# Optimization experiments

Hardware: AMD Instinct MI355X
Metric: run time of the kernel (lower is better)

## Reference

```python
import jax, jax.numpy as jnp
import numpy as np

B, S, L, H, N_ITEMS = 16, 20, 64, 768, 50000  # sessions, max items/session, tokens/item, hidden, catalog
T = S * L
TEMP = 0.05       # config.temp
PAD_POS = 50      # pad item position id (see torch code)
EPS = 1e-8        # torch CosineSimilarity eps


def setup_inputs() -> dict:
    key = jax.random.key(0)
    k1, k2, k3, k4 = jax.random.split(key, 4)
    hidden = jax.random.normal(k1, (B, T, H), jnp.float32)
    emb = jax.random.normal(k2, (N_ITEMS, H), jnp.float32)
    # item position ids: each item's L tokens share position 1..S; padded items -> 50
    pos = np.tile(np.repeat(np.arange(1, S + 1), L)[None, :], (B, 1))  # [B,T]
    sess_len = np.asarray(jax.random.randint(k3, (B,), S // 2, S + 1))  # items per session
    item_idx = np.repeat(np.arange(S), L)[None, :]                      # [1,T]
    pos = np.where(item_idx < sess_len[:, None], pos, PAD_POS).astype(np.int32)
    attn = (pos != PAD_POS).astype(np.int32)
    attrs = np.asarray(jax.random.randint(k4, (B, T), 0, 4)).astype(np.int32)
    return {
        "hidden_states": hidden,
        "item_embedding": emb,
        "attention_mask": jnp.asarray(attn),
        "item_position_ids": jnp.asarray(pos),
        "attr_type_ids": jnp.asarray(attrs),
    }


def reference(hidden_states, item_embedding, attention_mask, item_position_ids, attr_type_ids):
    # --- RecformerPooler (pooler_type='item'): nan-mean pool tokens per item ---
    item_ids = jnp.arange(1, S + 1, dtype=item_position_ids.dtype)
    mask = item_position_ids[:, None, :] == item_ids[None, :, None]      # [B,S,T]
    counts = mask.sum(-1)                                                # [B,S]
    valid = counts > 0                                                   # items present in session
    maskf = mask.astype(hidden_states.dtype)
    pooled = jnp.einsum('bst,bth->bsh', maskf, hidden_states)
    pooled = pooled / jnp.maximum(counts, 1)[..., None].astype(hidden_states.dtype)
    # (torch produces NaN rows for invalid items; we carry `valid` instead)

    # --- Similarity: cosine / temp vs full item catalog ---
    pn = jnp.maximum(jnp.linalg.norm(pooled, axis=-1, keepdims=True), EPS)
    en = jnp.maximum(jnp.linalg.norm(item_embedding, axis=-1, keepdims=True), EPS)
    sim = jnp.einsum('bsh,nh->bns', pooled / pn, item_embedding / en) / TEMP  # [B,N,S]

    # --- reduce_session('maxsim'): NaN -> -inf, max over session items ---
    sim = jnp.where(valid[:, None, :], sim, -jnp.inf)
    scores = sim.max(axis=-1)  # [B, N]; trailing mean over attr dim (size 1) is identity
    return scores
```

## Files before the change

kernel.cpp:

```cpp
#include <hip/hip_runtime.h>

#define B_ 16
#define S_ 20
#define L_ 64
#define T_ 1280
#define H_ 768
#define NITEMS 50000
#define TEMP 0.05f
#define EPSN 1e-8f

#define BM 320
#define BN 128
#define BK 32
#define NKT (H_ / BK)

typedef __attribute__((ext_vector_type(8))) short short8;
typedef __attribute__((ext_vector_type(4))) short short4v;
typedef __attribute__((ext_vector_type(4))) float f32x4;

__device__ __forceinline__ unsigned short f2bf(float f) {
    unsigned int u = __float_as_uint(f);
    u = u + 0x7FFFu + ((u >> 16) & 1u);
    return (unsigned short)(u >> 16);
}

typedef __attribute__((address_space(3))) void lds_void;
typedef const __attribute__((address_space(1))) void gbl_void;
__device__ __forceinline__ void load_lds16(const void* g, void* l) {
    __builtin_amdgcn_global_load_lds((gbl_void*)g, (lds_void*)l, 16, 0, 0);
}

__global__ __launch_bounds__(192) void pool_kernel(const float* __restrict__ hidden,
                                                   const int* __restrict__ pos,
                                                   unsigned short* __restrict__ A,
                                                   int* __restrict__ valid) {
    const int row = blockIdx.x;
    const int b = row / S_, s = row % S_;
    const int tid = threadIdx.x;

    __shared__ float wgt[L_];
    __shared__ int cntS;
    __shared__ float red[3];

    const int* pbase = pos + b * T_ + s * L_;
    if (tid < L_) {
        const int match = (pbase[tid] == s + 1) ? 1 : 0;
        unsigned long long bal = __ballot(match);
        wgt[tid] = match ? 1.0f : 0.0f;
        if (tid == 0) cntS = (int)__popcll(bal);
    }
    __syncthreads();

    const int cnt = cntS;
    const float inv = 1.0f / (float)(cnt > 0 ? cnt : 1);
    const float* hbase = hidden + ((size_t)b * T_ + (size_t)s * L_) * H_ + tid * 4;

    float a0 = 0.f, a1 = 0.f, a2 = 0.f, a3 = 0.f;
#pragma unroll 8
    for (int t = 0; t < L_; ++t) {
        const float w = wgt[t];
        const float4 v = *reinterpret_cast<const float4*>(hbase + (size_t)t * H_);
        a0 += w * v.x; a1 += w * v.y; a2 += w * v.z; a3 += w * v.w;
    }
    a0 *= inv; a1 *= inv; a2 *= inv; a3 *= inv;

    float ss = a0 * a0 + a1 * a1 + a2 * a2 + a3 * a3;
#pragma unroll
    for (int off = 32; off; off >>= 1) ss += __shfl_xor(ss, off, 64);
    const int wave = tid >> 6, lane = tid & 63;
    if (lane == 0) red[wave] = ss;
    __syncthreads();
    const float tot = red[0] + red[1] + red[2];
    const float scale = 1.0f / (fmaxf(sqrtf(tot), EPSN) * TEMP);

    short4v w4;
    w4[0] = (short)f2bf(a0 * scale);
    w4[1] = (short)f2bf(a1 * scale);
    w4[2] = (short)f2bf(a2 * scale);
    w4[3] = (short)f2bf(a3 * scale);
    *reinterpret_cast<short4v*>(A + (size_t)row * H_ + tid * 4) = w4;
    if (tid == 0) valid[row] = (cnt > 0) ? 1 : 0;
}

__global__ __launch_bounds__(256, 2) void gemm_kernel(const float* __restrict__ emb,
                                                      const unsigned short* __restrict__ A,
                                                      const int* __restrict__ valid,
                                                      float* __restrict__ out) {
    const int n0 = blockIdx.x * BN;
    const int tid = threadIdx.x;
    const int wave = tid >> 6, lane = tid & 63, quad = lane >> 4, lq = lane & 15;

    __shared__ alignas(16) short As[2][BM * BK];
    __shared__ alignas(16) float Bs[2][BN * BK];
    __shared__ float sEn[BN];
    __shared__ int sMask[B_];

    if (tid < B_) {
        int m = 0;
        for (int s = 0; s < S_; ++s) m |= (valid[tid * S_ + s] ? 1 : 0) << s;
        sMask[tid] = m;
    }

    const unsigned short* aSrc = A + (size_t)(tid >> 2) * H_ + (tid & 3) * 8;
    const float* bSrc[4];
#pragma unroll
    for (int i = 0; i < 4; ++i) {
        int r = n0 + (tid >> 3) + i * 32;
        if (r > NITEMS - 1) r = NITEMS - 1;
        bSrc[i] = emb + (size_t)r * H_ + (tid & 7) * 4;
    }

#pragma unroll
    for (int i = 0; i < 5; ++i)
        load_lds16(aSrc + i * 64 * H_, (char*)(&As[0][0]) + tid * 16 + i * 4096);
#pragma unroll
    for (int i = 0; i < 4; ++i)
        load_lds16(bSrc[i], (char*)(&Bs[0][0]) + tid * 16 + i * 4096);

    float rowSq = 0.f;
    f32x4 acc[20][2];
#pragma unroll
    for (int i = 0; i < 20; ++i) {
        acc[i][0] = (f32x4)0.f;
        acc[i][1] = (f32x4)0.f;
    }

    int cur = 0;
    for (int kt = 0; kt < NKT; ++kt) {
        __syncthreads();
        if (kt + 1 < NKT) {
            const int k0 = (kt + 1) * BK;
#pragma unroll
            for (int i = 0; i < 5; ++i)
                load_lds16(aSrc + k0 + i * 64 * H_,
                           (char*)(&As[cur ^ 1][0]) + tid * 16 + i * 4096);
#pragma unroll
            for (int i = 0; i < 4; ++i)
                load_lds16(bSrc[i] + k0,
                           (char*)(&Bs[cur ^ 1][0]) + tid * 16 + i * 4096);
        }

        {
            const float* ep = &Bs[cur][(tid >> 1) * BK + (tid & 1) * 16];
#pragma unroll
            for (int i = 0; i < 4; ++i) {
                const float4 v = *reinterpret_cast<const float4*>(ep + i * 4);
                rowSq += v.x * v.x + v.y * v.y + v.z * v.z + v.w * v.w;
            }
        }

        short8 bF[2];
#pragma unroll
        for (int nf = 0; nf < 2; ++nf) {
            const float* bp = &Bs[cur][(wave * 32 + nf * 16 + lq) * BK + quad * 8];
            const float4 x = *reinterpret_cast<const float4*>(bp);
            const float4 y = *reinterpret_cast<const float4*>(bp + 4);
            short8 f;
            f[0] = (short)f2bf(x.x); f[1] = (short)f2bf(x.y);
            f[2] = (short)f2bf(x.z); f[3] = (short)f2bf(x.w);
            f[4] = (short)f2bf(y.x); f[5] = (short)f2bf(y.y);
            f[6] = (short)f2bf(y.z); f[7] = (short)f2bf(y.w);
            bF[nf] = f;
        }

#pragma unroll
        for (int mf = 0; mf < 20; ++mf) {
            const short8 aF =
                *reinterpret_cast<const short8*>(&As[cur][(mf * 16 + lq) * BK + quad * 8]);
            acc[mf][0] = __builtin_amdgcn_mfma_f32_16x16x32_bf16(aF, bF[0], acc[mf][0], 0, 0, 0);
            acc[mf][1] = __builtin_amdgcn_mfma_f32_16x16x32_bf16(aF, bF[1], acc[mf][1], 0, 0, 0);
        }
        cur ^= 1;
    }

    rowSq += __shfl_xor(rowSq, 1, 64);
    if (!(tid & 1)) sEn[tid >> 1] = fmaxf(sqrtf(rowSq), EPSN);
    __syncthreads();

#pragma unroll
    for (int nf = 0; nf < 2; ++nf) {
        const int ncol = wave * 32 + nf * 16 + lq;
        const int n = n0 + ncol;
        if (n >= NITEMS) continue;
        const float inv_en = 1.0f / sEn[ncol];
#pragma unroll
        for (int bb = 0; bb < B_; ++bb) {
            const int rLo = bb * S_;
            const int msk = sMask[bb];
            float lm = -__builtin_inff();
            const int mfLo = rLo >> 4;
            const int mfHi = (rLo + S_ - 1) >> 4;
#pragma unroll
            for (int mf = mfLo; mf <= mfHi; ++mf)
#pragma unroll
                for (int e = 0; e < 4; ++e) {
                    const int r = mf * 16 + quad * 4 + e;
                    const unsigned off = (unsigned)(r - rLo);
                    const bool ok = (off < (unsigned)S_) && ((msk >> off) & 1);
                    lm = ok ? fmaxf(lm, acc[mf][nf][e]) : lm;
                }
            lm = fmaxf(lm, __shfl_xor(lm, 16, 64));
            lm = fmaxf(lm, __shfl_xor(lm, 32, 64));
            if (quad == 0)
                out[(size_t)bb * NITEMS + n] = lm * inv_en;
        }
    }
}

extern "C" void kernel_launch(void* const* d_in, const int* in_sizes, int n_in,
                              void* d_out, int out_size, void* d_ws, size_t ws_size,
                              hipStream_t stream) {
    const float* hidden = (const float*)d_in[0];
    const float* emb    = (const float*)d_in[1];
    const int*   pos    = (const int*)d_in[3];
    float* out = (float*)d_out;

    unsigned short* Abf = (unsigned short*)d_ws;
    int* valid = (int*)((char*)d_ws + (size_t)320 * 768 * 2);

    pool_kernel<<<dim3(320), dim3(192), 0, stream>>>(hidden, pos, Abf, valid);
    gemm_kernel<<<dim3((NITEMS + BN - 1) / BN), dim3(256), 0, stream>>>(emb, Abf, valid, out);
}
```

Before: 299.0 us.

## Halve N tile, convert embeddings to bf16 before LDS, split waves over M

The embedding tile now goes through registers: each thread loads fp32 values, adds them to the row norm, converts them to bf16 and writes them to LDS, prefetching one k-step ahead. Before, fp32 was copied straight to LDS and each wave converted its fragments on every use. BN drops from 128 to 64 and the wave decomposition changes from splitting N to splitting M (80 rows per wave, 5x4 fragments), so each wave handles 4 sessions in the epilogue. This cuts LDS footprint and per-thread conversion work and doubles the number of blocks. In exchange, A-tile reuse per embedding row is lower and the synchronous global loads now sit in the main loop.

```diff
diff --git a/kernel.cpp b/kernel.cpp
--- a/kernel.cpp
+++ b/kernel.cpp
@@ -10,7 +10,7 @@
 #define EPSN 1e-8f
 
 #define BM 320
-#define BN 128
+#define BN 64
 #define BK 32
 #define NKT (H_ / BK)
 
@@ -91,7 +91,7 @@
     const int wave = tid >> 6, lane = tid & 63, quad = lane >> 4, lq = lane & 15;
 
     __shared__ alignas(16) short As[2][BM * BK];
-    __shared__ alignas(16) float Bs[2][BN * BK];
+    __shared__ alignas(16) short Bs[2][BN * BK];
     __shared__ float sEn[BN];
     __shared__ int sMask[B_];
 
@@ -102,28 +102,38 @@
     }
 
     const unsigned short* aSrc = A + (size_t)(tid >> 2) * H_ + (tid & 3) * 8;
-    const float* bSrc[4];
-#pragma unroll
-    for (int i = 0; i < 4; ++i) {
-        int r = n0 + (tid >> 3) + i * 32;
-        if (r > NITEMS - 1) r = NITEMS - 1;
-        bSrc[i] = emb + (size_t)r * H_ + (tid & 7) * 4;
-    }
+
+    const int bRow = tid >> 2, bCol = (tid & 3) * 8;
+    int gr = n0 + bRow;
+    if (gr > NITEMS - 1) gr = NITEMS - 1;
+    const float* bPtr = emb + (size_t)gr * H_ + bCol;
+    const int bLds = bRow * BK + bCol;
 
 #pragma unroll
     for (int i = 0; i < 5; ++i)
         load_lds16(aSrc + i * 64 * H_, (char*)(&As[0][0]) + tid * 16 + i * 4096);
-#pragma unroll
-    for (int i = 0; i < 4; ++i)
-        load_lds16(bSrc[i], (char*)(&Bs[0][0]) + tid * 16 + i * 4096);
 
     float rowSq = 0.f;
-    f32x4 acc[20][2];
-#pragma unroll
-    for (int i = 0; i < 20; ++i) {
-        acc[i][0] = (f32x4)0.f;
-        acc[i][1] = (f32x4)0.f;
-    }
+    float4 c0 = *reinterpret_cast<const float4*>(bPtr);
+    float4 c1 = *reinterpret_cast<const float4*>(bPtr + 4);
+    {
+        rowSq += c0.x * c0.x + c0.y * c0.y + c0.z * c0.z + c0.w * c0.w;
+        rowSq += c1.x * c1.x + c1.y * c1.y + c1.z * c1.z + c1.w * c1.w;
+        short8 w;
+        w[0] = (short)f2bf(c0.x); w[1] = (short)f2bf(c0.y);
+        w[2] = (short)f2bf(c0.z); w[3] = (short)f2bf(c0.w);
+        w[4] = (short)f2bf(c1.x); w[5] = (short)f2bf(c1.y);
+        w[6] = (short)f2bf(c1.z); w[7] = (short)f2bf(c1.w);
+        *reinterpret_cast<short8*>(&Bs[0][bLds]) = w;
+    }
+    c0 = *reinterpret_cast<const float4*>(bPtr + BK);
+    c1 = *reinterpret_cast<const float4*>(bPtr + BK + 4);
+
+    f32x4 acc[5][4];
+#pragma unroll
+    for (int i = 0; i < 5; ++i)
+#pragma unroll
+        for (int j = 0; j < 4; ++j) acc[i][j] = (f32x4)0.f;
 
     int cur = 0;
     for (int kt = 0; kt < NKT; ++kt) {
@@ -134,62 +144,53 @@
             for (int i = 0; i < 5; ++i)
                 load_lds16(aSrc + k0 + i * 64 * H_,
                            (char*)(&As[cur ^ 1][0]) + tid * 16 + i * 4096);
-#pragma unroll
-            for (int i = 0; i < 4; ++i)
-                load_lds16(bSrc[i] + k0,
-                           (char*)(&Bs[cur ^ 1][0]) + tid * 16 + i * 4096);
-        }
-
-        {
-            const float* ep = &Bs[cur][(tid >> 1) * BK + (tid & 1) * 16];
-#pragma unroll
-            for (int i = 0; i < 4; ++i) {
-                const float4 v = *reinterpret_cast<const float4*>(ep + i * 4);
-                rowSq += v.x * v.x + v.y * v.y + v.z * v.z + v.w * v.w;
+            rowSq += c0.x * c0.x + c0.y * c0.y + c0.z * c0.z + c0.w * c0.w;
+            rowSq += c1.x * c1.x + c1.y * c1.y + c1.z * c1.z + c1.w * c1.w;
+            short8 w;
+            w[0] = (short)f2bf(c0.x); w[1] = (short)f2bf(c0.y);
+            w[2] = (short)f2bf(c0.z); w[3] = (short)f2bf(c0.w);
+            w[4] = (short)f2bf(c1.x); w[5] = (short)f2bf(c1.y);
+            w[6] = (short)f2bf(c1.z); w[7] = (short)f2bf(c1.w);
+            *reinterpret_cast<short8*>(&Bs[cur ^ 1][bLds]) = w;
+            if (kt + 2 < NKT) {
+                c0 = *reinterpret_cast<const float4*>(bPtr + (kt + 2) * BK);
+                c1 = *reinterpret_cast<const float4*>(bPtr + (kt + 2) * BK + 4);
             }
         }
 
-        short8 bF[2];
-#pragma unroll
-        for (int nf = 0; nf < 2; ++nf) {
-            const float* bp = &Bs[cur][(wave * 32 + nf * 16 + lq) * BK + quad * 8];
-            const float4 x = *reinterpret_cast<const float4*>(bp);
-            const float4 y = *reinterpret_cast<const float4*>(bp + 4);
-            short8 f;
-            f[0] = (short)f2bf(x.x); f[1] = (short)f2bf(x.y);
-            f[2] = (short)f2bf(x.z); f[3] = (short)f2bf(x.w);
-            f[4] = (short)f2bf(y.x); f[5] = (short)f2bf(y.y);
-            f[6] = (short)f2bf(y.z); f[7] = (short)f2bf(y.w);
-            bF[nf] = f;
-        }
-
-#pragma unroll
-        for (int mf = 0; mf < 20; ++mf) {
-            const short8 aF =
-                *reinterpret_cast<const short8*>(&As[cur][(mf * 16 + lq) * BK + quad * 8]);
-            acc[mf][0] = __builtin_amdgcn_mfma_f32_16x16x32_bf16(aF, bF[0], acc[mf][0], 0, 0, 0);
-            acc[mf][1] = __builtin_amdgcn_mfma_f32_16x16x32_bf16(aF, bF[1], acc[mf][1], 0, 0, 0);
+        short8 bF[4];
+#pragma unroll
+        for (int nf = 0; nf < 4; ++nf)
+            bF[nf] = *reinterpret_cast<const short8*>(&Bs[cur][(nf * 16 + lq) * BK + quad * 8]);
+
+#pragma unroll
+        for (int mf = 0; mf < 5; ++mf) {
+            const short8 aF = *reinterpret_cast<const short8*>(
+                &As[cur][(wave * 80 + mf * 16 + lq) * BK + quad * 8]);
+#pragma unroll
+            for (int nf = 0; nf < 4; ++nf)
+                acc[mf][nf] = __builtin_amdgcn_mfma_f32_16x16x32_bf16(aF, bF[nf], acc[mf][nf], 0, 0, 0);
         }
         cur ^= 1;
     }
 
     rowSq += __shfl_xor(rowSq, 1, 64);
-    if (!(tid & 1)) sEn[tid >> 1] = fmaxf(sqrtf(rowSq), EPSN);
+    rowSq += __shfl_xor(rowSq, 2, 64);
+    if ((tid & 3) == 0) sEn[bRow] = fmaxf(sqrtf(rowSq), EPSN);
     __syncthreads();
 
 #pragma unroll
-    for (int nf = 0; nf < 2; ++nf) {
-        const int ncol = wave * 32 + nf * 16 + lq;
+    for (int nf = 0; nf < 4; ++nf) {
+        const int ncol = nf * 16 + lq;
         const int n = n0 + ncol;
-        if (n >= NITEMS) continue;
         const float inv_en = 1.0f / sEn[ncol];
 #pragma unroll
-        for (int bb = 0; bb < B_; ++bb) {
+        for (int bb = 0; bb < 4; ++bb) {
             const int rLo = bb * S_;
-            const int msk = sMask[bb];
-            float lm = -__builtin_inff();
+            const int msk = sMask[wave * 4 + bb];
             const int mfLo = rLo >> 4;
             const int mfHi = (rLo + S_ - 1) >> 4;
+            float lm = -__builtin_inff();
 #pragma unroll
             for (int mf = mfLo; mf <= mfHi; ++mf)
 #pragma unroll
@@ -201,8 +202,8 @@
                 }
             lm = fmaxf(lm, __shfl_xor(lm, 16, 64));
             lm = fmaxf(lm, __shfl_xor(lm, 32, 64));
-            if (quad == 0)
-                out[(size_t)bb * NITEMS + n] = lm * inv_en;
+            if (quad == 0 && n < NITEMS)
+                out[(size_t)(wave * 4 + bb) * NITEMS + n] = lm * inv_en;
         }
     }
 }
```

After: 307.7 us. +2.9%, slower.

## Split GEMM over session groups, keep A resident in LDS, stream embeddings from registers

Applied to the files above, without the earlier changes.

The GEMM now runs on a 2D grid: each block holds an 80-row slice of the pooled matrix (4 sessions) fully in padded LDS and covers 256 catalog items with 8 waves. Each wave loads its embedding rows straight from global into registers, converts them to bf16 with a cheaper pack, and computes the row norms with shuffles. This drops the double-buffered LDS staging and most per-iteration barriers and cuts accumulator registers, which should raise occupancy. The cost is that the fp32 embedding matrix is read four times, once per session group, relying on L2 for reuse, and global load latency is no longer hidden by async prefetch. The bf16 rounding changes from round-to-nearest-even to round-half-up.

```diff
diff --git a/kernel.cpp b/kernel.cpp
--- a/kernel.cpp
+++ b/kernel.cpp
@@ -9,14 +9,14 @@
 #define TEMP 0.05f
 #define EPSN 1e-8f
 
-#define BM 320
-#define BN 128
-#define BK 32
-#define NKT (H_ / BK)
+#define MT 80
+#define ROWPAD 776
+#define NKT 24
 
 typedef __attribute__((ext_vector_type(8))) short short8;
 typedef __attribute__((ext_vector_type(4))) short short4v;
 typedef __attribute__((ext_vector_type(4))) float f32x4;
+typedef __attribute__((ext_vector_type(4))) unsigned int u32x4;
 
 __device__ __forceinline__ unsigned short f2bf(float f) {
     unsigned int u = __float_as_uint(f);
@@ -24,10 +24,10 @@
     return (unsigned short)(u >> 16);
 }
 
-typedef __attribute__((address_space(3))) void lds_void;
-typedef const __attribute__((address_space(1))) void gbl_void;
-__device__ __forceinline__ void load_lds16(const void* g, void* l) {
-    __builtin_amdgcn_global_load_lds((gbl_void*)g, (lds_void*)l, 16, 0, 0);
+__device__ __forceinline__ unsigned int pack_bf16(float f0, float f1) {
+    const unsigned int u0 = __float_as_uint(f0) + 0x8000u;
+    const unsigned int u1 = __float_as_uint(f1) + 0x8000u;
+    return __builtin_amdgcn_perm(u1, u0, 0x07060302u);
 }
 
 __global__ __launch_bounds__(192) void pool_kernel(const float* __restrict__ hidden,
@@ -82,114 +82,98 @@
     if (tid == 0) valid[row] = (cnt > 0) ? 1 : 0;
 }
 
-__global__ __launch_bounds__(256, 2) void gemm_kernel(const float* __restrict__ emb,
+__global__ __launch_bounds__(512, 2) void gemm_kernel(const float* __restrict__ emb,
                                                       const unsigned short* __restrict__ A,
                                                       const int* __restrict__ valid,
                                                       float* __restrict__ out) {
-    const int n0 = blockIdx.x * BN;
+    const int mt = blockIdx.x;
+    const int nt = blockIdx.y;
     const int tid = threadIdx.x;
     const int wave = tid >> 6, lane = tid & 63, quad = lane >> 4, lq = lane & 15;
 
-    __shared__ alignas(16) short As[2][BM * BK];
-    __shared__ alignas(16) float Bs[2][BN * BK];
-    __shared__ float sEn[BN];
-    __shared__ int sMask[B_];
-
-    if (tid < B_) {
+    __shared__ alignas(16) short As[MT * ROWPAD];
+    __shared__ int sMask[4];
+
+    if (tid < 4) {
         int m = 0;
-        for (int s = 0; s < S_; ++s) m |= (valid[tid * S_ + s] ? 1 : 0) << s;
+        for (int s = 0; s < S_; ++s) m |= (valid[(mt * 4 + tid) * S_ + s] ? 1 : 0) << s;
         sMask[tid] = m;
     }
 
-    const unsigned short* aSrc = A + (size_t)(tid >> 2) * H_ + (tid & 3) * 8;
-    const float* bSrc[4];
-#pragma unroll
-    for (int i = 0; i < 4; ++i) {
-        int r = n0 + (tid >> 3) + i * 32;
-        if (r > NITEMS - 1) r = NITEMS - 1;
-        bSrc[i] = emb + (size_t)r * H_ + (tid & 7) * 4;
-    }
-
-#pragma unroll
-    for (int i = 0; i < 5; ++i)
-        load_lds16(aSrc + i * 64 * H_, (char*)(&As[0][0]) + tid * 16 + i * 4096);
-#pragma unroll
-    for (int i = 0; i < 4; ++i)
-        load_lds16(bSrc[i], (char*)(&Bs[0][0]) + tid * 16 + i * 4096);
-
-    float rowSq = 0.f;
-    f32x4 acc[20][2];
-#pragma unroll
-    for (int i = 0; i < 20; ++i) {
+    const unsigned short* Ab = A + (size_t)(mt * MT) * H_;
+#pragma unroll
+    for (int i = 0; i < 15; ++i) {
+        const int c = i * 512 + tid;
+        const int r = c / 96, cc = c % 96;
+        const u32x4 v = *reinterpret_cast<const u32x4*>(Ab + r * H_ + cc * 8);
+        *reinterpret_cast<u32x4*>(reinterpret_cast<char*>(As) + r * (ROWPAD * 2) + cc * 16) = v;
+    }
+    __syncthreads();
+
+    const int n0w = nt * 256 + wave * 32;
+    int r0 = n0w + lq;        if (r0 > NITEMS - 1) r0 = NITEMS - 1;
+    int r1 = n0w + 16 + lq;   if (r1 > NITEMS - 1) r1 = NITEMS - 1;
+    const float* bp0 = emb + (size_t)r0 * H_ + quad * 8;
+    const float* bp1 = emb + (size_t)r1 * H_ + quad * 8;
+
+    const short* aBase[5];
+#pragma unroll
+    for (int mf = 0; mf < 5; ++mf)
+        aBase[mf] = &As[(mf * 16 + lq) * ROWPAD + quad * 8];
+
+    float rowSq0 = 0.f, rowSq1 = 0.f;
+    f32x4 acc[5][2];
+#pragma unroll
+    for (int i = 0; i < 5; ++i) {
         acc[i][0] = (f32x4)0.f;
         acc[i][1] = (f32x4)0.f;
     }
 
-    int cur = 0;
+#pragma unroll 8
     for (int kt = 0; kt < NKT; ++kt) {
-        __syncthreads();
-        if (kt + 1 < NKT) {
-            const int k0 = (kt + 1) * BK;
-#pragma unroll
-            for (int i = 0; i < 5; ++i)
-                load_lds16(aSrc + k0 + i * 64 * H_,
-                           (char*)(&As[cur ^ 1][0]) + tid * 16 + i * 4096);
-#pragma unroll
-            for (int i = 0; i < 4; ++i)
-                load_lds16(bSrc[i] + k0,
-                           (char*)(&Bs[cur ^ 1][0]) + tid * 16 + i * 4096);
+        const float4 x0 = *reinterpret_cast<const float4*>(bp0 + kt * 32);
+        const float4 y0 = *reinterpret_cast<const float4*>(bp0 + kt * 32 + 4);
+        const float4 x1 = *reinterpret_cast<const float4*>(bp1 + kt * 32);
+        const float4 y1 = *reinterpret_cast<const float4*>(bp1 + kt * 32 + 4);
+
+        rowSq0 += x0.x * x0.x + x0.y * x0.y + x0.z * x0.z + x0.w * x0.w
+                + y0.x * y0.x + y0.y * y0.y + y0.z * y0.z + y0.w * y0.w;
+        rowSq1 += x1.x * x1.x + x1.y * x1.y + x1.z * x1.z + x1.w * x1.w
+                + y1.x * y1.x + y1.y * y1.y + y1.z * y1.z + y1.w * y1.w;
+
+        union { short8 s; u32x4 u; } bF0, bF1;
+        bF0.u[0] = pack_bf16(x0.x, x0.y); bF0.u[1] = pack_bf16(x0.z, x0.w);
+        bF0.u[2] = pack_bf16(y0.x, y0.y); bF0.u[3] = pack_bf16(y0.z, y0.w);
+        bF1.u[0] = pack_bf16(x1.x, x1.y); bF1.u[1] = pack_bf16(x1.z, x1.w);
+        bF1.u[2] = pack_bf16(y1.x, y1.y); bF1.u[3] = pack_bf16(y1.z, y1.w);
+
+#pragma unroll
+        for (int mf = 0; mf < 5; ++mf) {
+            const short8 aF = *reinterpret_cast<const short8*>(aBase[mf] + kt * 32);
+            acc[mf][0] = __builtin_amdgcn_mfma_f32_16x16x32_bf16(aF, bF0.s, acc[mf][0], 0, 0, 0);
+            acc[mf][1] = __builtin_amdgcn_mfma_f32_16x16x32_bf16(aF, bF1.s, acc[mf][1], 0, 0, 0);
         }
-
-        {
-            const float* ep = &Bs[cur][(tid >> 1) * BK + (tid & 1) * 16];
-#pragma unroll
-            for (int i = 0; i < 4; ++i) {
-                const float4 v = *reinterpret_cast<const float4*>(ep + i * 4);
-                rowSq += v.x * v.x + v.y * v.y + v.z * v.z + v.w * v.w;
-            }
-        }
-
-        short8 bF[2];
-#pragma unroll
-        for (int nf = 0; nf < 2; ++nf) {
-            const float* bp = &Bs[cur][(wave * 32 + nf * 16 + lq) * BK + quad * 8];
-            const float4 x = *reinterpret_cast<const float4*>(bp);
-            const float4 y = *reinterpret_cast<const float4*>(bp + 4);
-            short8 f;
-            f[0] = (short)f2bf(x.x); f[1] = (short)f2bf(x.y);
-            f[2] = (short)f2bf(x.z); f[3] = (short)f2bf(x.w);
-            f[4] = (short)f2bf(y.x); f[5] = (short)f2bf(y.y);
-            f[6] = (short)f2bf(y.z); f[7] = (short)f2bf(y.w);
-            bF[nf] = f;
-        }
-
-#pragma unroll
-        for (int mf = 0; mf < 20; ++mf) {
-            const short8 aF =
-                *reinterpret_cast<const short8*>(&As[cur][(mf * 16 + lq) * BK + quad * 8]);
-            acc[mf][0] = __builtin_amdgcn_mfma_f32_16x16x32_bf16(aF, bF[0], acc[mf][0], 0, 0, 0);
-            acc[mf][1] = __builtin_amdgcn_mfma_f32_16x16x32_bf16(aF, bF[1], acc[mf][1], 0, 0, 0);
-        }
-        cur ^= 1;
-    }
-
-    rowSq += __shfl_xor(rowSq, 1, 64);
-    if (!(tid & 1)) sEn[tid >> 1] = fmaxf(sqrtf(rowSq), EPSN);
-    __syncthreads();
+    }
+
+    rowSq0 += __shfl_xor(rowSq0, 16, 64);
+    rowSq0 += __shfl_xor(rowSq0, 32, 64);
+    rowSq1 += __shfl_xor(rowSq1, 16, 64);
+    rowSq1 += __shfl_xor(rowSq1, 32, 64);
+    float invEn[2];
+    invEn[0] = 1.0f / fmaxf(sqrtf(rowSq0), EPSN);
+    invEn[1] = 1.0f / fmaxf(sqrtf(rowSq1), EPSN);
 
 #pragma unroll
     for (int nf = 0; nf < 2; ++nf) {
-        const int ncol = wave * 32 + nf * 16 + lq;
-        const int n = n0 + ncol;
-        if (n >= NITEMS) continue;
-        const float inv_en = 1.0f / sEn[ncol];
-#pragma unroll
-        for (int bb = 0; bb < B_; ++bb) {
+        const int n = n0w + nf * 16 + lq;
+        const float inv_en = invEn[nf];
+#pragma unroll
+        for (int bb = 0; bb < 4; ++bb) {
             const int rLo = bb * S_;
             const int msk = sMask[bb];
-            float lm = -__builtin_inff();
             const int mfLo = rLo >> 4;
             const int mfHi = (rLo + S_ - 1) >> 4;
+            float lm = -__builtin_inff();
 #pragma unroll
             for (int mf = mfLo; mf <= mfHi; ++mf)
 #pragma unroll
@@ -201,8 +185,8 @@
                 }
             lm = fmaxf(lm, __shfl_xor(lm, 16, 64));
             lm = fmaxf(lm, __shfl_xor(lm, 32, 64));
-            if (quad == 0)
-                out[(size_t)bb * NITEMS + n] = lm * inv_en;
+            if (quad == 0 && n < NITEMS)
+                out[(size_t)(mt * 4 + bb) * NITEMS + n] = lm * inv_en;
         }
     }
 }
@@ -219,5 +203,5 @@
     int* valid = (int*)((char*)d_ws + (size_t)320 * 768 * 2);
 
     pool_kernel<<<dim3(320), dim3(192), 0, stream>>>(hidden, pos, Abf, valid);
-    gemm_kernel<<<dim3((NITEMS + BN - 1) / BN), dim3(256), 0, stream>>>(emb, Abf, valid, out);
-}
+    gemm_kernel<<<dim3(4, 196), dim3(512), 0, stream>>>(emb, Abf, valid, out);
+}
```

Measured after the change: 344.4 us. 1.15x slower.
